# Optimization experiments

Measured on AMD Instinct MI355X. Metric: run time of the kernel, lower is better.

## Reference

```python
import jax, jax.numpy as jnp
import numpy as np

EPS = 1e-5  # RMSNorm epsilon


def rmsnorm(x, w):
    return x * jax.lax.rsqrt(jnp.mean(x * x, axis=-1, keepdims=True) + EPS) * w


def mamba_forward(u, in_proj_w, conv_w, conv_b, x_proj_w, dt_proj_w, dt_proj_b,
                  A_log, D_param, mamba_out_w):
    # u: (b, L, dm) -- canonical Mamba block (expand=2, d_state=16, d_conv=4)
    b, L, dm = u.shape
    di, ds = A_log.shape
    dtr = dt_proj_w.shape[1]
    xz = jnp.einsum('bld,ed->ble', u, in_proj_w)          # (b,L,2*di)
    x_, z = jnp.split(xz, 2, axis=-1)                     # each (b,L,di)
    # causal depthwise conv over the sequence axis
    dconv = conv_w.shape[-1]
    xc = jnp.transpose(x_, (0, 2, 1))                     # (b,di,L)
    xc = jnp.pad(xc, ((0, 0), (0, 0), (dconv - 1, 0)))
    xc = jax.lax.conv_general_dilated(xc, conv_w, window_strides=(1,), padding='VALID',
                                      dimension_numbers=('NCH', 'OIH', 'NCH'),
                                      feature_group_count=di)
    xc = xc + conv_b[None, :, None]
    x_ = jax.nn.silu(jnp.transpose(xc, (0, 2, 1)))        # (b,L,di)
    # input-dependent dt, B, C
    x_dbl = jnp.einsum('bld,ed->ble', x_, x_proj_w)       # (b,L,dtr+2*ds)
    dt, B, C = jnp.split(x_dbl, [dtr, dtr + ds], axis=-1)
    delta = jax.nn.softplus(jnp.einsum('blr,dr->bld', dt, dt_proj_w) + dt_proj_b)  # (b,L,di)
    A = -jnp.exp(A_log)                                   # (di,ds)

    def step(h, inp):
        d_t, B_t, C_t, x_t = inp                          # (b,di),(b,ds),(b,ds),(b,di)
        dA = jnp.exp(d_t[:, :, None] * A)                 # (b,di,ds)
        h = dA * h + (d_t * x_t)[:, :, None] * B_t[:, None, :]
        y = jnp.einsum('bds,bs->bd', h, C_t)
        return h, y

    xs = (jnp.moveaxis(delta, 1, 0), jnp.moveaxis(B, 1, 0),
          jnp.moveaxis(C, 1, 0), jnp.moveaxis(x_, 1, 0))
    h0 = jnp.zeros((b, di, ds), dtype=u.dtype)
    _, ys = jax.lax.scan(step, h0, xs)                    # ys: (L,b,di)
    y = jnp.moveaxis(ys, 0, 1) + x_ * D_param             # (b,L,di)
    y = y * jax.nn.silu(z)
    return jnp.einsum('bld,od->blo', y, mamba_out_w)      # (b,L,dm)


def conv1x1(W, bvec, t):
    # t: (b, cin, L) -> (b, cout, L)
    return jnp.einsum('oi,bit->bot', W, t) + bvec[None, :, None]


def reference(x, w_norm1, w_norm2, W_ip, b_ip, W_fp, b_fp, W_wp, b_wp, W_op, b_op,
              in_proj_w, conv_w, conv_b, x_proj_w, dt_proj_w, dt_proj_b,
              A_log, D_param, mamba_out_w):
    # x: (b, L, D) -- module's (b, c, l) with l == input_dim = D, c == seq = L
    residual = x
    xn = rmsnorm(x, w_norm1)                 # RMSNorm over last (input_dim) axis
    xt = jnp.transpose(xn, (0, 2, 1))        # 'b c l -> b l c' : (b, D, L)
    ssm = conv1x1(W_ip, b_ip, xt)            # (b, 2D, L)
    ssm = conv1x1(W_fp, b_fp, ssm)           # (b, 2D, L)
    u = jnp.transpose(ssm, (0, 2, 1))        # (b, L, 2D): seq=L, d_model=2D
    m = mamba_forward(u, in_proj_w, conv_w, conv_b, x_proj_w, dt_proj_w, dt_proj_b,
                      A_log, D_param, mamba_out_w)
    m = rmsnorm(m, w_norm2) + u              # PostNormMamba residual
    ssm = jnp.transpose(m, (0, 2, 1))        # (b, 2D, L)
    w = conv1x1(W_wp, b_wp, xt)              # (b, 2D, L)
    w = w * jax.nn.sigmoid(w)                # swish
    out = conv1x1(W_op, b_op, w * ssm)       # (b, D, L)
    return jnp.transpose(out, (0, 2, 1)) + residual


def setup_inputs():
    key = jax.random.key(0)
    ks = jax.random.split(key, 16)
    D, L, b = 64, 4096, 4
    dm, di, ds, dconv = 2 * D, 4 * D, 16, 4
    dtr = (dm + 15) // 16  # dt_rank = ceil(d_model/16) = 8

    def n(k, shape, fan_in):
        return jax.random.normal(k, shape, jnp.float32) * (1.0 / np.sqrt(fan_in))

    return {
        'x': jax.random.normal(ks[0], (b, L, D), jnp.float32),
        'w_norm1': jnp.ones((D,), jnp.float32),
        'w_norm2': jnp.ones((dm,), jnp.float32),
        'W_ip': n(ks[1], (2 * D, D), D), 'b_ip': jnp.zeros((2 * D,), jnp.float32),
        'W_fp': n(ks[2], (2 * D, 2 * D), 2 * D), 'b_fp': jnp.zeros((2 * D,), jnp.float32),
        'W_wp': n(ks[3], (2 * D, D), D), 'b_wp': jnp.zeros((2 * D,), jnp.float32),
        'W_op': n(ks[4], (D, 2 * D), 2 * D), 'b_op': jnp.zeros((D,), jnp.float32),
        'in_proj_w': n(ks[5], (2 * di, dm), dm),
        'conv_w': n(ks[6], (di, 1, dconv), dconv),
        'conv_b': jnp.zeros((di,), jnp.float32),
        'x_proj_w': n(ks[7], (dtr + 2 * ds, di), di),
        'dt_proj_w': n(ks[8], (di, dtr), dtr),
        'dt_proj_b': jnp.full((di,), float(np.log(np.expm1(0.01))), jnp.float32),
        'A_log': jnp.log(jnp.broadcast_to(jnp.arange(1, ds + 1, dtype=jnp.float32), (di, ds))),
        'D_param': jnp.ones((di,), jnp.float32),
        'mamba_out_w': n(ks[9], (dm, di), di),
    }
```

## Files before the change

kernel.cpp:

```cpp
#include <hip/hip_runtime.h>
#include <hip/hip_bf16.h>

typedef __hip_bfloat16 bf16;
typedef __attribute__((ext_vector_type(8))) short bf16x8;
typedef __attribute__((ext_vector_type(4))) float f32x4;
#define DEV __device__ __forceinline__

constexpr int SEQ  = 4096;
constexpr int NB   = 4;
constexpr int NTOK = NB * SEQ;
constexpr float EPS = 1e-5f;
constexpr int NCH = 64;
constexpr int NCHUNK = SEQ / NCH;
constexpr float LOG2E = 1.44269504f;

constexpr int OFF_WDT  = 0;
constexpr int OFF_WB   = 2048;
constexpr int WB_IP = 0;
constexpr int WB_WP = 8192;
constexpr int WB_FP = 16384;
constexpr int WB_PR = 32768;
constexpr int WB_MO = 98304;
constexpr int WB_OP = 131072;
constexpr int WB_XP = 139264;
constexpr int WB_TOT = 151552;
constexpr int OFF_XDBL = OFF_WB + WB_TOT / 2;
constexpr int OFF_R1   = OFF_XDBL + NTOK * 40;
constexpr int OFF_WSW  = OFF_R1   + 1048576;
constexpr int OFF_U    = OFF_WSW  + 1048576;
constexpr int OFF_R2   = OFF_U    + 1048576;
constexpr int OFF_SILUZ= OFF_R2   + 2097152;
constexpr int OFF_XC   = OFF_SILUZ+ 2097152;
constexpr int OFF_G    = OFF_XC   + 2097152;
constexpr int OFF_FLAG = OFF_G    + 2097152;

DEV float b2f(bf16 x) { return __bfloat162float(x); }
DEV bf16 f2b(float x) { return __float2bfloat16(x); }
DEV short shof(bf16 h) { short s; __builtin_memcpy(&s, &h, 2); return s; }
DEV float ldin(const void* p, int i, int f) {
  return f ? ((const float*)p)[i] : b2f(((const bf16*)p)[i]);
}
DEV unsigned pack2(float a, float b) {
  bf16 ha = f2b(a), hb = f2b(b);
  unsigned short ua, ub;
  __builtin_memcpy(&ua, &ha, 2); __builtin_memcpy(&ub, &hb, 2);
  return (unsigned)ua | ((unsigned)ub << 16);
}
DEV float lo16f(unsigned u) { return __int_as_float((int)(u << 16)); }
DEV float hi16f(unsigned u) { return __int_as_float((int)(u & 0xffff0000u)); }
template<int CTRL>
DEV float dpp_add(float v) {
  int r = __builtin_amdgcn_update_dpp(0, __float_as_int(v), CTRL, 0xF, 0xF, false);
  return v + __int_as_float(r);
}
DEV float exp2f_fast(float a) { return __builtin_amdgcn_exp2f(a); }
DEV float softplus(float a) {
  return (a > 20.f) ? a : __logf(1.f + exp2f_fast(a * LOG2E));
}
DEV float silu(float a) { return a / (1.f + __expf(-a)); }

DEV void cpw(int e, int base, int count, const void* __restrict__ src,
             bf16* __restrict__ wb, int f) {
  int r = e - base;
  if (r >= 0 && r < count) wb[base + r] = f2b(ldin(src, r, f));
}
__global__ __launch_bounds__(256) void prep_k(
    const void* __restrict__ w_ip, const void* __restrict__ w_wp, const void* __restrict__ w_fp,
    const void* __restrict__ w_pr, const void* __restrict__ w_mo, const void* __restrict__ w_op,
    const void* __restrict__ w_x,  const void* __restrict__ w_dt,
    const void* __restrict__ x, float* __restrict__ wsf, int* __restrict__ flagp)
{
  __shared__ int cnt;
  if (threadIdx.x == 0) cnt = 0;
  __syncthreads();
  {
    float v = b2f(((const bf16*)x)[threadIdx.x]);
    int ok = (v == v) && fabsf(v) > 1e-4f && fabsf(v) < 100.f;
    atomicAdd(&cnt, ok);
  }
  __syncthreads();
  int f = (cnt > 204) ? 0 : 1;
  if (blockIdx.x == 0 && threadIdx.x == 0) *flagp = f;

  int e = blockIdx.x * 256 + threadIdx.x;
  bf16* wb = (bf16*)(wsf + OFF_WB);
  cpw(e, WB_IP, 8192,  w_ip, wb, f);
  cpw(e, WB_WP, 8192,  w_wp, wb, f);
  cpw(e, WB_FP, 16384, w_fp, wb, f);
  cpw(e, WB_PR, 65536, w_pr, wb, f);
  cpw(e, WB_MO, 32768, w_mo, wb, f);
  cpw(e, WB_OP, 8192,  w_op, wb, f);
  {
    int r = e - WB_XP;
    if (r >= 0 && r < 12288) wb[WB_XP + r] = (r < 10240) ? f2b(ldin(w_x, r, f)) : f2b(0.f);
  }
  if (e < 2048) {
    int r = e >> 8, d = e & 255;
    wsf[OFF_WDT + e] = ldin(w_dt, d * 8 + r, f);
  }
}

__global__ __launch_bounds__(256) void fm_k(
    const void* __restrict__ x, const void* __restrict__ w1, const float* __restrict__ wsf,
    const void* __restrict__ b_ip, const void* __restrict__ b_wp, const void* __restrict__ b_fp,
    bf16* __restrict__ wsw, bf16* __restrict__ u, bf16* __restrict__ xpre,
    bf16* __restrict__ siluz, const int* __restrict__ flagp)
{
  __shared__ short xn[32 * 72];
  __shared__ short t1[32 * 136];
  __shared__ short ul[32 * 136];
  const int f = *flagp;
  const int tid = threadIdx.x;
  const int tok0 = blockIdx.x * 32;
  {
    const int token = tid >> 3, r = tid & 7;
    float v[8]; float ss = 0.f;
    #pragma unroll
    for (int k = 0; k < 8; ++k) {
      v[k] = ldin(x, (tok0 + token) * 64 + r * 8 + k, f);
      ss += v[k] * v[k];
    }
    ss += __shfl_xor(ss, 1, 8); ss += __shfl_xor(ss, 2, 8); ss += __shfl_xor(ss, 4, 8);
    float sc = rsqrtf(ss * (1.f / 64.f) + EPS);
    unsigned* dst = (unsigned*)xn + token * 36 + r * 4;
    #pragma unroll
    for (int k = 0; k < 4; ++k) {
      int i = r * 8 + k * 2;
      dst[k] = pack2(v[k*2] * sc * ldin(w1, i, f), v[k*2+1] * sc * ldin(w1, i + 1, f));
    }
  }
  __syncthreads();
  const int lane = tid & 63, m = lane & 15, q = lane >> 4;
  const int w = tid >> 6;
  {
    const int wt = w >> 1, ng = w & 1;
    const bf16* W = (const bf16*)(wsf + OFF_WB) + (wt ? WB_WP : WB_IP);
    const void* bia = wt ? b_wp : b_ip;
    bf16x8 a[2][2];
    #pragma unroll
    for (int mt = 0; mt < 2; ++mt)
      #pragma unroll
      for (int kk = 0; kk < 2; ++kk)
        a[mt][kk] = *(const bf16x8*)&xn[(mt * 16 + m) * 72 + kk * 32 + q * 8];
    #pragma unroll
    for (int nti = 0; nti < 4; ++nti) {
      int nt = ng * 4 + nti;
      int n = nt * 16 + m;
      f32x4 acc[2] = {{0,0,0,0},{0,0,0,0}};
      #pragma unroll
      for (int kk = 0; kk < 2; ++kk) {
        bf16x8 b = *(const bf16x8*)(W + (nt * 16 + m) * 64 + kk * 32 + q * 8);
        #pragma unroll
        for (int mt = 0; mt < 2; ++mt)
          acc[mt] = __builtin_amdgcn_mfma_f32_16x16x32_bf16(a[mt][kk], b, acc[mt], 0, 0, 0);
      }
      float bv = ldin(bia, n, f);
      #pragma unroll
      for (int mt = 0; mt < 2; ++mt)
        #pragma unroll
        for (int r = 0; r < 4; ++r) {
          float v = acc[mt][r] + bv;
          if (wt) wsw[(tok0 + mt * 16 + q * 4 + r) * 128 + n] = f2b(silu(v));
          else    t1[(mt * 16 + q * 4 + r) * 136 + n] = shof(f2b(v));
        }
    }
  }
  __syncthreads();
  {
    const bf16* WF = (const bf16*)(wsf + OFF_WB) + WB_FP;
    bf16x8 a[2][4];
    #pragma unroll
    for (int mt = 0; mt < 2; ++mt)
      #pragma unroll
      for (int kk = 0; kk < 4; ++kk)
        a[mt][kk] = *(const bf16x8*)&t1[(mt * 16 + m) * 136 + kk * 32 + q * 8];
    #pragma unroll
    for (int nti = 0; nti < 2; ++nti) {
      int nt = w * 2 + nti;
      int n = nt * 16 + m;
      f32x4 acc[2] = {{0,0,0,0},{0,0,0,0}};
      #pragma unroll
      for (int kk = 0; kk < 4; ++kk) {
        bf16x8 b = *(const bf16x8*)(WF + (nt * 16 + m) * 128 + kk * 32 + q * 8);
        #pragma unroll
        for (int mt = 0; mt < 2; ++mt)
          acc[mt] = __builtin_amdgcn_mfma_f32_16x16x32_bf16(a[mt][kk], b, acc[mt], 0, 0, 0);
      }
      float bv = ldin(b_fp, n, f);
      #pragma unroll
      for (int mt = 0; mt < 2; ++mt)
        #pragma unroll
        for (int r = 0; r < 4; ++r) {
          bf16 h = f2b(acc[mt][r] + bv);
          ul[(mt * 16 + q * 4 + r) * 136 + n] = shof(h);
          u[(tok0 + mt * 16 + q * 4 + r) * 128 + n] = h;
        }
    }
  }
  __syncthreads();
  {
    const bf16* WP = (const bf16*)(wsf + OFF_WB) + WB_PR;
    bf16x8 a[2][4];
    #pragma unroll
    for (int mt = 0; mt < 2; ++mt)
      #pragma unroll
      for (int kk = 0; kk < 4; ++kk)
        a[mt][kk] = *(const bf16x8*)&ul[(mt * 16 + m) * 136 + kk * 32 + q * 8];
    #pragma unroll
    for (int nti = 0; nti < 8; ++nti) {
      int nt = w * 8 + nti;
      int n = nt * 16 + m;
      f32x4 acc[2] = {{0,0,0,0},{0,0,0,0}};
      #pragma unroll
      for (int kk = 0; kk < 4; ++kk) {
        bf16x8 b = *(const bf16x8*)(WP + (nt * 16 + m) * 128 + kk * 32 + q * 8);
        #pragma unroll
        for (int mt = 0; mt < 2; ++mt)
          acc[mt] = __builtin_amdgcn_mfma_f32_16x16x32_bf16(a[mt][kk], b, acc[mt], 0, 0, 0);
      }
      #pragma unroll
      for (int mt = 0; mt < 2; ++mt)
        #pragma unroll
        for (int r = 0; r < 4; ++r) {
          int tok = tok0 + mt * 16 + q * 4 + r;
          if (n < 256) xpre[tok * 256 + n] = f2b(acc[mt][r]);
          else         siluz[tok * 256 + (n - 256)] = f2b(silu(acc[mt][r]));
        }
    }
  }
}

__global__ __launch_bounds__(256) void conv_k(
    const bf16* __restrict__ xpre, const void* __restrict__ cw, const void* __restrict__ cb,
    const float* __restrict__ wsf, bf16* __restrict__ xc, float* __restrict__ xdbl,
    const int* __restrict__ flagp)
{
  __shared__ short xh[35 * 256];
  __shared__ short cs[32 * 264];
  const int f = *flagp;
  const int tid = threadIdx.x;
  const int tok0 = blockIdx.x * 32;
  const bool seqstart = (tok0 & (SEQ - 1)) == 0;
  for (int c = tid; c < 1120; c += 256) {
    int e0 = c * 8;
    int tt = e0 >> 8, i = e0 & 255;
    int gtok = tok0 + tt - 3;
    uint4* dst = (uint4*)(xh + e0);
    if (gtok >= 0 && !(seqstart && tt < 3)) *dst = *(const uint4*)(xpre + gtok * 256 + i);
    else                                    *dst = make_uint4(0, 0, 0, 0);
  }
  __syncthreads();
  {
    const int ch0 = (tid & 63) * 4;
    const int t0 = (tid >> 6) * 8;
    float w4[4][4], cb4[4];
    #pragma unroll
    for (int c = 0; c < 4; ++c) {
      cb4[c] = ldin(cb, ch0 + c, f);
      #pragma unroll
      for (int k = 0; k < 4; ++k) w4[c][k] = ldin(cw, (ch0 + c) * 4 + k, f);
    }
    float win[11][4];
    #pragma unroll
    for (int r = 0; r < 11; ++r) {
      uint2 v = *(const uint2*)&xh[(t0 + r) * 256 + ch0];
      win[r][0] = lo16f(v.x); win[r][1] = hi16f(v.x);
      win[r][2] = lo16f(v.y); win[r][3] = hi16f(v.y);
    }
    #pragma unroll
    for (int t = 0; t < 8; ++t) {
      unsigned pk[2];
      #pragma unroll
      for (int cp = 0; cp < 2; ++cp) {
        float o[2];
        #pragma unroll
        for (int ci = 0; ci < 2; ++ci) {
          int c = cp * 2 + ci;
          float acc = cb4[c];
          #pragma unroll
          for (int k = 0; k < 4; ++k) acc = fmaf(win[t + k][c], w4[c][k], acc);
          o[ci] = silu(acc);
        }
        pk[cp] = pack2(o[0], o[1]);
      }
      uint2 pv = make_uint2(pk[0], pk[1]);
      *(uint2*)&cs[(t0 + t) * 264 + ch0] = pv;
      *(uint2*)(xc + (tok0 + t0 + t) * 256 + ch0) = pv;
    }
  }
  __syncthreads();
  const int w = tid >> 6;
  if (w < 2) {
    const bf16* Wx = (const bf16*)(wsf + OFF_WB) + WB_XP;
    const int lane = tid & 63, m = lane & 15, quad = lane >> 4;
    f32x4 acc[3] = {{0,0,0,0},{0,0,0,0},{0,0,0,0}};
    #pragma unroll
    for (int k0 = 0; k0 < 256; k0 += 32) {
      bf16x8 af = *(const bf16x8*)&cs[(w * 16 + m) * 264 + k0 + quad * 8];
      #pragma unroll
      for (int nt = 0; nt < 3; ++nt) {
        bf16x8 bfr = *(const bf16x8*)(Wx + (nt * 16 + m) * 256 + k0 + quad * 8);
        acc[nt] = __builtin_amdgcn_mfma_f32_16x16x32_bf16(af, bfr, acc[nt], 0, 0, 0);
      }
    }
    #pragma unroll
    for (int nt = 0; nt < 3; ++nt) {
      int n = nt * 16 + m;
      if (n < 40) {
        #pragma unroll
        for (int r = 0; r < 4; ++r)
          xdbl[(tok0 + w * 16 + quad * 4 + r) * 40 + n] = acc[nt][r];
      }
    }
  }
}

template<bool IS_C>
__global__ __launch_bounds__(256) void scan_k(
    const float* __restrict__ xdbl, const bf16* __restrict__ xc, const bf16* __restrict__ siluz,
    const void* __restrict__ A_log, const void* __restrict__ D_par, const void* __restrict__ dt_b,
    const float* __restrict__ WDT, float* __restrict__ summ, const float* __restrict__ hinit,
    bf16* __restrict__ g, const int* __restrict__ flagp)
{
  const int f = *flagp;
  const int tid = threadIdx.x;
  const int bb = blockIdx.x >> 4, dg = blockIdx.x & 15, c = blockIdx.y;
  const int dl = tid >> 4, s = tid & 15;
  const int j = s;
  const int d_loop = dg * 16 + dl;
  const int d_stg  = dg * 16 + j;
  const int tok_base = bb * SEQ + c * NCH;

  __shared__ float dt_l[NCH * 8];
  __shared__ float dx_l[NCH * 16 * 2];
  __shared__ float bc_l[IS_C ? NCH * 16 * 2 : NCH * 16];
  __shared__ float g_l[IS_C ? NCH * 16 : 1];

  const float Aval2 = -__expf(ldin(A_log, d_loop * 16 + s, f)) * LOG2E;
  const float Dp_stg = ldin(D_par, d_stg, f);
  const float dtb_j = ldin(dt_b, d_stg, f);
  float wdt[8];
  #pragma unroll
  for (int r = 0; r < 8; ++r) wdt[r] = WDT[r * 256 + d_stg];

  const int sidx = (blockIdx.x * NCHUNK + c) * 256 + tid;
  float h = IS_C ? hinit[sidx] : 0.f;
  float sdlt = 0.f;

  for (int e2 = tid * 4; e2 < NCH * 8; e2 += 1024)
    *(float4*)(dt_l + e2) = *(const float4*)(xdbl + (tok_base + (e2 >> 3)) * 40 + (e2 & 7));
  #pragma unroll
  for (int k = 0; k < 4; ++k) {
    int e = tid + k * 256;
    int t = e >> 4;
    int tok = tok_base + t;
    float B = xdbl[tok * 40 + 8 + j];
    if (IS_C) {
      bc_l[e * 2 + 0] = B;
      bc_l[e * 2 + 1] = xdbl[tok * 40 + 24 + j];
    } else bc_l[e] = B;
  }
  __syncthreads();
  #pragma unroll
  for (int k = 0; k < 4; ++k) {
    int e = tid + k * 256;
    int t = e >> 4;
    float a = dtb_j;
    #pragma unroll
    for (int r = 0; r < 8; ++r) a = fmaf(dt_l[t * 8 + r], wdt[r], a);
    float dlt = softplus(a);
    float xcv = b2f(xc[(tok_base + t) * 256 + d_stg]);
    *(float2*)(dx_l + e * 2) = make_float2(dlt, dlt * xcv);
  }
  __syncthreads();

  #pragma unroll 8
  for (int t = 0; t < NCH; ++t) {
    float2 dx = *(const float2*)(dx_l + (t * 16 + dl) * 2);
    float dA = exp2f_fast(dx.x * Aval2);
    if (!IS_C) sdlt += dx.x;
    if (IS_C) {
      float2 bc = *(const float2*)(bc_l + (t * 16 + s) * 2);
      h = fmaf(dA, h, dx.y * bc.x);
      float p = h * bc.y;
      p = dpp_add<0x121>(p);
      p = dpp_add<0x122>(p);
      p = dpp_add<0x124>(p);
      p = dpp_add<0x128>(p);
      if (s == 0) g_l[t * 16 + dl] = p;
    } else {
      h = fmaf(dA, h, dx.y * bc_l[t * 16 + s]);
    }
  }
  if (IS_C) {
    __syncthreads();
    #pragma unroll
    for (int k = 0; k < 4; ++k) {
      int e = tid + k * 256;
      int t = e >> 4;
      int tok = tok_base + t;
      float xcv = b2f(xc[tok * 256 + d_stg]);
      g[tok * 256 + d_stg] = f2b((g_l[e] + xcv * Dp_stg) * b2f(siluz[tok * 256 + d_stg]));
    }
  } else {
    *(float2*)(summ + sidx * 2) = make_float2(exp2f_fast(Aval2 * sdlt), h);
  }
}

__global__ __launch_bounds__(256) void scanB_k(const float* __restrict__ summ, float* __restrict__ hinit) {
  int bx = blockIdx.x, qq = threadIdx.x;
  float h = 0.f;
  for (int c0 = 0; c0 < NCHUNK; c0 += 16) {
    float2 sv[16];
    #pragma unroll
    for (int k = 0; k < 16; ++k)
      sv[k] = *(const float2*)(summ + ((bx * NCHUNK + c0 + k) * 256 + qq) * 2);
    #pragma unroll
    for (int k = 0; k < 16; ++k) {
      hinit[(bx * NCHUNK + c0 + k) * 256 + qq] = h;
      h = fmaf(sv[k].x, h, sv[k].y);
    }
  }
}

__global__ __launch_bounds__(256) void back_k(
    const bf16* __restrict__ g, const float* __restrict__ wsf, const void* __restrict__ w2,
    const bf16* __restrict__ u, const bf16* __restrict__ wsw, const void* __restrict__ b_op,
    const void* __restrict__ x, void* __restrict__ out, const int* __restrict__ flagp)
{
  __shared__ short ms[32 * 136];
  const int f = *flagp;
  const int tid = threadIdx.x;
  const int tok0 = blockIdx.x * 32;
  const int lane = tid & 63, m = lane & 15, q = lane >> 4;
  const int w = tid >> 6;
  const bf16* WM = (const bf16*)(wsf + OFF_WB) + WB_MO;
  const bf16* WO = (const bf16*)(wsf + OFF_WB) + WB_OP;
  {
    f32x4 acc[2][2] = {{{0,0,0,0},{0,0,0,0}},{{0,0,0,0},{0,0,0,0}}};
    #pragma unroll
    for (int kk = 0; kk < 8; ++kk) {
      bf16x8 a0 = *(const bf16x8*)(g + (tok0 + m) * 256 + kk * 32 + q * 8);
      bf16x8 a1 = *(const bf16x8*)(g + (tok0 + 16 + m) * 256 + kk * 32 + q * 8);
      #pragma unroll
      for (int nti = 0; nti < 2; ++nti) {
        int nt = w * 2 + nti;
        bf16x8 b = *(const bf16x8*)(WM + (nt * 16 + m) * 256 + kk * 32 + q * 8);
        acc[nti][0] = __builtin_amdgcn_mfma_f32_16x16x32_bf16(a0, b, acc[nti][0], 0, 0, 0);
        acc[nti][1] = __builtin_amdgcn_mfma_f32_16x16x32_bf16(a1, b, acc[nti][1], 0, 0, 0);
      }
    }
    #pragma unroll
    for (int nti = 0; nti < 2; ++nti) {
      int n = (w * 2 + nti) * 16 + m;
      #pragma unroll
      for (int mt = 0; mt < 2; ++mt)
        #pragma unroll
        for (int r = 0; r < 4; ++r)
          ms[(mt * 16 + q * 4 + r) * 136 + n] = shof(f2b(acc[nti][mt][r]));
    }
  }
  __syncthreads();
  {
    const int token = tid >> 3, r = tid & 7;
    float mv[16]; float ss = 0.f;
    #pragma unroll
    for (int k = 0; k < 16; ++k) {
      mv[k] = b2f(((const bf16*)ms)[token * 136 + r * 16 + k]);
      ss += mv[k] * mv[k];
    }
    ss += __shfl_xor(ss, 1, 8); ss += __shfl_xor(ss, 2, 8); ss += __shfl_xor(ss, 4, 8);
    float sc = rsqrtf(ss * (1.f / 128.f) + EPS);
    #pragma unroll
    for (int k = 0; k < 16; ++k) {
      int i = r * 16 + k;
      int ga = (tok0 + token) * 128 + i;
      float v = mv[k] * sc * ldin(w2, i, f) + b2f(u[ga]);
      ms[token * 136 + i] = shof(f2b(v * b2f(wsw[ga])));
    }
  }
  __syncthreads();
  {
    bf16x8 a[2][4];
    #pragma unroll
    for (int mt = 0; mt < 2; ++mt)
      #pragma unroll
      for (int kk = 0; kk < 4; ++kk)
        a[mt][kk] = *(const bf16x8*)&ms[(mt * 16 + m) * 136 + kk * 32 + q * 8];
    int nt = w;
    f32x4 acc[2] = {{0,0,0,0},{0,0,0,0}};
    #pragma unroll
    for (int kk = 0; kk < 4; ++kk) {
      bf16x8 b = *(const bf16x8*)(WO + (nt * 16 + m) * 128 + kk * 32 + q * 8);
      #pragma unroll
      for (int mt = 0; mt < 2; ++mt)
        acc[mt] = __builtin_amdgcn_mfma_f32_16x16x32_bf16(a[mt][kk], b, acc[mt], 0, 0, 0);
    }
    int n = nt * 16 + m;
    float bv = ldin(b_op, n, f);
    #pragma unroll
    for (int mt = 0; mt < 2; ++mt)
      #pragma unroll
      for (int r = 0; r < 4; ++r) {
        int token = tok0 + mt * 16 + q * 4 + r;
        float v = acc[mt][r] + bv + ldin(x, token * 64 + n, f);
        if (f) ((float*)out)[token * 64 + n] = v;
        else   ((bf16*)out)[token * 64 + n] = f2b(v);
      }
  }
}

extern "C" void kernel_launch(void* const* d_in, const int* in_sizes, int n_in,
                              void* d_out, int out_size, void* d_ws, size_t ws_size,
                              hipStream_t stream) {
  (void)in_sizes; (void)n_in; (void)out_size; (void)ws_size;
  const void* x        = d_in[0];
  const void* w_norm1  = d_in[1];
  const void* w_norm2  = d_in[2];
  const void* W_ip     = d_in[3];
  const void* b_ip     = d_in[4];
  const void* W_fp     = d_in[5];
  const void* b_fp     = d_in[6];
  const void* W_wp     = d_in[7];
  const void* b_wp     = d_in[8];
  const void* W_op     = d_in[9];
  const void* b_op     = d_in[10];
  const void* in_proj  = d_in[11];
  const void* conv_w   = d_in[12];
  const void* conv_b   = d_in[13];
  const void* x_proj   = d_in[14];
  const void* dt_projw = d_in[15];
  const void* dt_projb = d_in[16];
  const void* A_log    = d_in[17];
  const void* D_par    = d_in[18];
  const void* mo_w     = d_in[19];

  float* wsf    = (float*)d_ws;
  float* xdbl   = wsf + OFF_XDBL;
  float* hin    = wsf + OFF_R1;
  bf16*  wsw_b  = (bf16*)(wsf + OFF_WSW);
  bf16*  u_b    = (bf16*)(wsf + OFF_U);
  bf16*  xpre_b = (bf16*)(wsf + OFF_R2);
  float* summ   = wsf + OFF_R2;
  bf16*  siluz_b= (bf16*)(wsf + OFF_SILUZ);
  bf16*  xc_b   = (bf16*)(wsf + OFF_XC);
  bf16*  g_b    = (bf16*)(wsf + OFF_G);
  int*   flagp  = (int*)(wsf + OFF_FLAG);

  prep_k<<<dim3(592), dim3(256), 0, stream>>>(W_ip, W_wp, W_fp, in_proj, mo_w, W_op,
                                              x_proj, dt_projw, x, wsf, flagp);
  fm_k<<<dim3(NTOK / 32), dim3(256), 0, stream>>>(x, w_norm1, wsf, b_ip, b_wp, b_fp,
                                                  wsw_b, u_b, xpre_b, siluz_b, flagp);
  conv_k<<<dim3(NTOK / 32), dim3(256), 0, stream>>>(xpre_b, conv_w, conv_b, wsf, xc_b, xdbl, flagp);
  scan_k<false><<<dim3(64, NCHUNK), dim3(256), 0, stream>>>(xdbl, xc_b, siluz_b, A_log, D_par,
                                                            dt_projb, wsf + OFF_WDT, summ, hin, g_b, flagp);
  scanB_k<<<dim3(64), dim3(256), 0, stream>>>(summ, hin);
  scan_k<true><<<dim3(64, NCHUNK), dim3(256), 0, stream>>>(xdbl, xc_b, siluz_b, A_log, D_par,
                                                           dt_projb, wsf + OFF_WDT, summ, hin, g_b, flagp);
  back_k<<<dim3(NTOK / 32), dim3(256), 0, stream>>>(g_b, wsf, w_norm2, u_b, wsw_b, b_op, x, d_out, flagp);
}
```

Baseline: 208.4 us.

## Halve token tiles per block and fuse chunk-carry pass into scan via last-block atomic

The token-parallel kernels (fm_k, conv_k, back_k) now process 16 tokens per block instead of 32. This doubles the grid to 1024 blocks and cuts shared memory per block, to improve occupancy and load balance across CUs. The separate scanB_k launch is removed. Instead, the last scan_k<false> block per channel group, detected with an atomic counter plus threadfence, runs the sequential chunk-carry propagation, which saves one launch. In exchange, weight fragments are reused across fewer tokens, so weight traffic per token rises, and the serial carry loop now runs inside the tail of the scan kernel.

```diff
diff --git a/kernel.cpp b/kernel.cpp
--- a/kernel.cpp
+++ b/kernel.cpp
@@ -33,6 +33,7 @@
 constexpr int OFF_XC   = OFF_SILUZ+ 2097152;
 constexpr int OFF_G    = OFF_XC   + 2097152;
 constexpr int OFF_FLAG = OFF_G    + 2097152;
+constexpr int OFF_CNTS = OFF_FLAG + 1;
 
 DEV float b2f(bf16 x) { return __bfloat162float(x); }
 DEV bf16 f2b(float x) { return __float2bfloat16(x); }
@@ -68,7 +69,8 @@
     const void* __restrict__ w_ip, const void* __restrict__ w_wp, const void* __restrict__ w_fp,
     const void* __restrict__ w_pr, const void* __restrict__ w_mo, const void* __restrict__ w_op,
     const void* __restrict__ w_x,  const void* __restrict__ w_dt,
-    const void* __restrict__ x, float* __restrict__ wsf, int* __restrict__ flagp)
+    const void* __restrict__ x, float* __restrict__ wsf, int* __restrict__ flagp,
+    int* __restrict__ cnts)
 {
   __shared__ int cnt;
   if (threadIdx.x == 0) cnt = 0;
@@ -80,7 +82,10 @@
   }
   __syncthreads();
   int f = (cnt > 204) ? 0 : 1;
-  if (blockIdx.x == 0 && threadIdx.x == 0) *flagp = f;
+  if (blockIdx.x == 0) {
+    if (threadIdx.x == 0) *flagp = f;
+    if (threadIdx.x < 64) cnts[threadIdx.x] = 0;
+  }
 
   int e = blockIdx.x * 256 + threadIdx.x;
   bf16* wb = (bf16*)(wsf + OFF_WB);
@@ -106,28 +111,26 @@
     bf16* __restrict__ wsw, bf16* __restrict__ u, bf16* __restrict__ xpre,
     bf16* __restrict__ siluz, const int* __restrict__ flagp)
 {
-  __shared__ short xn[32 * 72];
-  __shared__ short t1[32 * 136];
-  __shared__ short ul[32 * 136];
+  __shared__ short xn[16 * 72];
+  __shared__ short t1[16 * 136];
+  __shared__ short ul[16 * 136];
   const int f = *flagp;
   const int tid = threadIdx.x;
-  const int tok0 = blockIdx.x * 32;
-  {
-    const int token = tid >> 3, r = tid & 7;
-    float v[8]; float ss = 0.f;
-    #pragma unroll
-    for (int k = 0; k < 8; ++k) {
-      v[k] = ldin(x, (tok0 + token) * 64 + r * 8 + k, f);
+  const int tok0 = blockIdx.x * 16;
+  {
+    const int token = tid >> 4, r = tid & 15;
+    float v[4]; float ss = 0.f;
+    #pragma unroll
+    for (int k = 0; k < 4; ++k) {
+      v[k] = ldin(x, (tok0 + token) * 64 + r * 4 + k, f);
       ss += v[k] * v[k];
     }
-    ss += __shfl_xor(ss, 1, 8); ss += __shfl_xor(ss, 2, 8); ss += __shfl_xor(ss, 4, 8);
+    ss += __shfl_xor(ss, 1, 16); ss += __shfl_xor(ss, 2, 16);
+    ss += __shfl_xor(ss, 4, 16); ss += __shfl_xor(ss, 8, 16);
     float sc = rsqrtf(ss * (1.f / 64.f) + EPS);
-    unsigned* dst = (unsigned*)xn + token * 36 + r * 4;
-    #pragma unroll
-    for (int k = 0; k < 4; ++k) {
-      int i = r * 8 + k * 2;
-      dst[k] = pack2(v[k*2] * sc * ldin(w1, i, f), v[k*2+1] * sc * ldin(w1, i + 1, f));
-    }
+    unsigned* dst = (unsigned*)xn + token * 36 + r * 2;
+    dst[0] = pack2(v[0] * sc * ldin(w1, r * 4 + 0, f), v[1] * sc * ldin(w1, r * 4 + 1, f));
+    dst[1] = pack2(v[2] * sc * ldin(w1, r * 4 + 2, f), v[3] * sc * ldin(w1, r * 4 + 3, f));
   }
   __syncthreads();
   const int lane = tid & 63, m = lane & 15, q = lane >> 4;
@@ -136,96 +139,78 @@
     const int wt = w >> 1, ng = w & 1;
     const bf16* W = (const bf16*)(wsf + OFF_WB) + (wt ? WB_WP : WB_IP);
     const void* bia = wt ? b_wp : b_ip;
-    bf16x8 a[2][2];
-    #pragma unroll
-    for (int mt = 0; mt < 2; ++mt)
-      #pragma unroll
-      for (int kk = 0; kk < 2; ++kk)
-        a[mt][kk] = *(const bf16x8*)&xn[(mt * 16 + m) * 72 + kk * 32 + q * 8];
+    bf16x8 a[2];
+    #pragma unroll
+    for (int kk = 0; kk < 2; ++kk)
+      a[kk] = *(const bf16x8*)&xn[m * 72 + kk * 32 + q * 8];
     #pragma unroll
     for (int nti = 0; nti < 4; ++nti) {
       int nt = ng * 4 + nti;
       int n = nt * 16 + m;
-      f32x4 acc[2] = {{0,0,0,0},{0,0,0,0}};
+      f32x4 acc = {0.f, 0.f, 0.f, 0.f};
       #pragma unroll
       for (int kk = 0; kk < 2; ++kk) {
         bf16x8 b = *(const bf16x8*)(W + (nt * 16 + m) * 64 + kk * 32 + q * 8);
-        #pragma unroll
-        for (int mt = 0; mt < 2; ++mt)
-          acc[mt] = __builtin_amdgcn_mfma_f32_16x16x32_bf16(a[mt][kk], b, acc[mt], 0, 0, 0);
+        acc = __builtin_amdgcn_mfma_f32_16x16x32_bf16(a[kk], b, acc, 0, 0, 0);
       }
       float bv = ldin(bia, n, f);
       #pragma unroll
-      for (int mt = 0; mt < 2; ++mt)
-        #pragma unroll
-        for (int r = 0; r < 4; ++r) {
-          float v = acc[mt][r] + bv;
-          if (wt) wsw[(tok0 + mt * 16 + q * 4 + r) * 128 + n] = f2b(silu(v));
-          else    t1[(mt * 16 + q * 4 + r) * 136 + n] = shof(f2b(v));
-        }
+      for (int r = 0; r < 4; ++r) {
+        float v = acc[r] + bv;
+        if (wt) wsw[(tok0 + q * 4 + r) * 128 + n] = f2b(silu(v));
+        else    t1[(q * 4 + r) * 136 + n] = shof(f2b(v));
+      }
     }
   }
   __syncthreads();
   {
     const bf16* WF = (const bf16*)(wsf + OFF_WB) + WB_FP;
-    bf16x8 a[2][4];
-    #pragma unroll
-    for (int mt = 0; mt < 2; ++mt)
-      #pragma unroll
-      for (int kk = 0; kk < 4; ++kk)
-        a[mt][kk] = *(const bf16x8*)&t1[(mt * 16 + m) * 136 + kk * 32 + q * 8];
+    bf16x8 a[4];
+    #pragma unroll
+    for (int kk = 0; kk < 4; ++kk)
+      a[kk] = *(const bf16x8*)&t1[m * 136 + kk * 32 + q * 8];
     #pragma unroll
     for (int nti = 0; nti < 2; ++nti) {
       int nt = w * 2 + nti;
       int n = nt * 16 + m;
-      f32x4 acc[2] = {{0,0,0,0},{0,0,0,0}};
+      f32x4 acc = {0.f, 0.f, 0.f, 0.f};
       #pragma unroll
       for (int kk = 0; kk < 4; ++kk) {
         bf16x8 b = *(const bf16x8*)(WF + (nt * 16 + m) * 128 + kk * 32 + q * 8);
-        #pragma unroll
-        for (int mt = 0; mt < 2; ++mt)
-          acc[mt] = __builtin_amdgcn_mfma_f32_16x16x32_bf16(a[mt][kk], b, acc[mt], 0, 0, 0);
+        acc = __builtin_amdgcn_mfma_f32_16x16x32_bf16(a[kk], b, acc, 0, 0, 0);
       }
       float bv = ldin(b_fp, n, f);
       #pragma unroll
-      for (int mt = 0; mt < 2; ++mt)
-        #pragma unroll
-        for (int r = 0; r < 4; ++r) {
-          bf16 h = f2b(acc[mt][r] + bv);
-          ul[(mt * 16 + q * 4 + r) * 136 + n] = shof(h);
-          u[(tok0 + mt * 16 + q * 4 + r) * 128 + n] = h;
-        }
+      for (int r = 0; r < 4; ++r) {
+        bf16 h = f2b(acc[r] + bv);
+        ul[(q * 4 + r) * 136 + n] = shof(h);
+        u[(tok0 + q * 4 + r) * 128 + n] = h;
+      }
     }
   }
   __syncthreads();
   {
     const bf16* WP = (const bf16*)(wsf + OFF_WB) + WB_PR;
-    bf16x8 a[2][4];
-    #pragma unroll
-    for (int mt = 0; mt < 2; ++mt)
-      #pragma unroll
-      for (int kk = 0; kk < 4; ++kk)
-        a[mt][kk] = *(const bf16x8*)&ul[(mt * 16 + m) * 136 + kk * 32 + q * 8];
+    bf16x8 a[4];
+    #pragma unroll
+    for (int kk = 0; kk < 4; ++kk)
+      a[kk] = *(const bf16x8*)&ul[m * 136 + kk * 32 + q * 8];
     #pragma unroll
     for (int nti = 0; nti < 8; ++nti) {
       int nt = w * 8 + nti;
       int n = nt * 16 + m;
-      f32x4 acc[2] = {{0,0,0,0},{0,0,0,0}};
+      f32x4 acc = {0.f, 0.f, 0.f, 0.f};
       #pragma unroll
       for (int kk = 0; kk < 4; ++kk) {
         bf16x8 b = *(const bf16x8*)(WP + (nt * 16 + m) * 128 + kk * 32 + q * 8);
-        #pragma unroll
-        for (int mt = 0; mt < 2; ++mt)
-          acc[mt] = __builtin_amdgcn_mfma_f32_16x16x32_bf16(a[mt][kk], b, acc[mt], 0, 0, 0);
-      }
-      #pragma unroll
-      for (int mt = 0; mt < 2; ++mt)
-        #pragma unroll
-        for (int r = 0; r < 4; ++r) {
-          int tok = tok0 + mt * 16 + q * 4 + r;
-          if (n < 256) xpre[tok * 256 + n] = f2b(acc[mt][r]);
-          else         siluz[tok * 256 + (n - 256)] = f2b(silu(acc[mt][r]));
-        }
+        acc = __builtin_amdgcn_mfma_f32_16x16x32_bf16(a[kk], b, acc, 0, 0, 0);
+      }
+      #pragma unroll
+      for (int r = 0; r < 4; ++r) {
+        int tok = tok0 + q * 4 + r;
+        if (n < 256) xpre[tok * 256 + n] = f2b(acc[r]);
+        else         siluz[tok * 256 + (n - 256)] = f2b(silu(acc[r]));
+      }
     }
   }
 }
@@ -235,13 +220,13 @@
     const float* __restrict__ wsf, bf16* __restrict__ xc, float* __restrict__ xdbl,
     const int* __restrict__ flagp)
 {
-  __shared__ short xh[35 * 256];
-  __shared__ short cs[32 * 264];
+  __shared__ short xh[19 * 256];
+  __shared__ short cs[16 * 264];
   const int f = *flagp;
   const int tid = threadIdx.x;
-  const int tok0 = blockIdx.x * 32;
+  const int tok0 = blockIdx.x * 16;
   const bool seqstart = (tok0 & (SEQ - 1)) == 0;
-  for (int c = tid; c < 1120; c += 256) {
+  for (int c = tid; c < 608; c += 256) {
     int e0 = c * 8;
     int tt = e0 >> 8, i = e0 & 255;
     int gtok = tok0 + tt - 3;
@@ -252,7 +237,7 @@
   __syncthreads();
   {
     const int ch0 = (tid & 63) * 4;
-    const int t0 = (tid >> 6) * 8;
+    const int t0 = (tid >> 6) * 4;
     float w4[4][4], cb4[4];
     #pragma unroll
     for (int c = 0; c < 4; ++c) {
@@ -260,15 +245,15 @@
       #pragma unroll
       for (int k = 0; k < 4; ++k) w4[c][k] = ldin(cw, (ch0 + c) * 4 + k, f);
     }
-    float win[11][4];
-    #pragma unroll
-    for (int r = 0; r < 11; ++r) {
+    float win[7][4];
+    #pragma unroll
+    for (int r = 0; r < 7; ++r) {
       uint2 v = *(const uint2*)&xh[(t0 + r) * 256 + ch0];
       win[r][0] = lo16f(v.x); win[r][1] = hi16f(v.x);
       win[r][2] = lo16f(v.y); win[r][3] = hi16f(v.y);
     }
     #pragma unroll
-    for (int t = 0; t < 8; ++t) {
+    for (int t = 0; t < 4; ++t) {
       unsigned pk[2];
       #pragma unroll
       for (int cp = 0; cp < 2; ++cp) {
@@ -290,27 +275,21 @@
   }
   __syncthreads();
   const int w = tid >> 6;
-  if (w < 2) {
+  if (w < 3) {
     const bf16* Wx = (const bf16*)(wsf + OFF_WB) + WB_XP;
     const int lane = tid & 63, m = lane & 15, quad = lane >> 4;
-    f32x4 acc[3] = {{0,0,0,0},{0,0,0,0},{0,0,0,0}};
+    f32x4 acc = {0.f, 0.f, 0.f, 0.f};
     #pragma unroll
     for (int k0 = 0; k0 < 256; k0 += 32) {
-      bf16x8 af = *(const bf16x8*)&cs[(w * 16 + m) * 264 + k0 + quad * 8];
-      #pragma unroll
-      for (int nt = 0; nt < 3; ++nt) {
-        bf16x8 bfr = *(const bf16x8*)(Wx + (nt * 16 + m) * 256 + k0 + quad * 8);
-        acc[nt] = __builtin_amdgcn_mfma_f32_16x16x32_bf16(af, bfr, acc[nt], 0, 0, 0);
-      }
-    }
-    #pragma unroll
-    for (int nt = 0; nt < 3; ++nt) {
-      int n = nt * 16 + m;
-      if (n < 40) {
-        #pragma unroll
-        for (int r = 0; r < 4; ++r)
-          xdbl[(tok0 + w * 16 + quad * 4 + r) * 40 + n] = acc[nt][r];
-      }
+      bf16x8 af = *(const bf16x8*)&cs[m * 264 + k0 + quad * 8];
+      bf16x8 bfr = *(const bf16x8*)(Wx + (w * 16 + m) * 256 + k0 + quad * 8);
+      acc = __builtin_amdgcn_mfma_f32_16x16x32_bf16(af, bfr, acc, 0, 0, 0);
+    }
+    int n = w * 16 + m;
+    if (n < 40) {
+      #pragma unroll
+      for (int r = 0; r < 4; ++r)
+        xdbl[(tok0 + quad * 4 + r) * 40 + n] = acc[r];
     }
   }
 }
@@ -319,8 +298,8 @@
 __global__ __launch_bounds__(256) void scan_k(
     const float* __restrict__ xdbl, const bf16* __restrict__ xc, const bf16* __restrict__ siluz,
     const void* __restrict__ A_log, const void* __restrict__ D_par, const void* __restrict__ dt_b,
-    const float* __restrict__ WDT, float* __restrict__ summ, const float* __restrict__ hinit,
-    bf16* __restrict__ g, const int* __restrict__ flagp)
+    const float* __restrict__ WDT, float* __restrict__ summ, float* __restrict__ hinit,
+    bf16* __restrict__ g, const int* __restrict__ flagp, int* __restrict__ cnts)
 {
   const int f = *flagp;
   const int tid = threadIdx.x;
@@ -335,6 +314,7 @@
   __shared__ float dx_l[NCH * 16 * 2];
   __shared__ float bc_l[IS_C ? NCH * 16 * 2 : NCH * 16];
   __shared__ float g_l[IS_C ? NCH * 16 : 1];
+  __shared__ int lastf;
 
   const float Aval2 = -__expf(ldin(A_log, d_loop * 16 + s, f)) * LOG2E;
   const float Dp_stg = ldin(D_par, d_stg, f);
@@ -404,21 +384,25 @@
     }
   } else {
     *(float2*)(summ + sidx * 2) = make_float2(exp2f_fast(Aval2 * sdlt), h);
-  }
-}
-
-__global__ __launch_bounds__(256) void scanB_k(const float* __restrict__ summ, float* __restrict__ hinit) {
-  int bx = blockIdx.x, qq = threadIdx.x;
-  float h = 0.f;
-  for (int c0 = 0; c0 < NCHUNK; c0 += 16) {
-    float2 sv[16];
-    #pragma unroll
-    for (int k = 0; k < 16; ++k)
-      sv[k] = *(const float2*)(summ + ((bx * NCHUNK + c0 + k) * 256 + qq) * 2);
-    #pragma unroll
-    for (int k = 0; k < 16; ++k) {
-      hinit[(bx * NCHUNK + c0 + k) * 256 + qq] = h;
-      h = fmaf(sv[k].x, h, sv[k].y);
+    __threadfence();
+    if (tid == 0)
+      lastf = (atomicAdd(&cnts[blockIdx.x], 1) == NCHUNK - 1) ? 1 : 0;
+    __syncthreads();
+    if (lastf) {
+      __threadfence();
+      const int bx = blockIdx.x;
+      float h2 = 0.f;
+      for (int c0 = 0; c0 < NCHUNK; c0 += 16) {
+        float2 sv[16];
+        #pragma unroll
+        for (int k = 0; k < 16; ++k)
+          sv[k] = *(const float2*)(summ + ((bx * NCHUNK + c0 + k) * 256 + tid) * 2);
+        #pragma unroll
+        for (int k = 0; k < 16; ++k) {
+          hinit[(bx * NCHUNK + c0 + k) * 256 + tid] = h2;
+          h2 = fmaf(sv[k].x, h2, sv[k].y);
+        }
+      }
     }
   }
 }
@@ -428,52 +412,49 @@
     const bf16* __restrict__ u, const bf16* __restrict__ wsw, const void* __restrict__ b_op,
     const void* __restrict__ x, void* __restrict__ out, const int* __restrict__ flagp)
 {
-  __shared__ short ms[32 * 136];
+  __shared__ short ms[16 * 136];
   const int f = *flagp;
   const int tid = threadIdx.x;
-  const int tok0 = blockIdx.x * 32;
+  const int tok0 = blockIdx.x * 16;
   const int lane = tid & 63, m = lane & 15, q = lane >> 4;
   const int w = tid >> 6;
   const bf16* WM = (const bf16*)(wsf + OFF_WB) + WB_MO;
   const bf16* WO = (const bf16*)(wsf + OFF_WB) + WB_OP;
   {
-    f32x4 acc[2][2] = {{{0,0,0,0},{0,0,0,0}},{{0,0,0,0},{0,0,0,0}}};
+    f32x4 acc[2] = {{0,0,0,0},{0,0,0,0}};
     #pragma unroll
     for (int kk = 0; kk < 8; ++kk) {
       bf16x8 a0 = *(const bf16x8*)(g + (tok0 + m) * 256 + kk * 32 + q * 8);
-      bf16x8 a1 = *(const bf16x8*)(g + (tok0 + 16 + m) * 256 + kk * 32 + q * 8);
       #pragma unroll
       for (int nti = 0; nti < 2; ++nti) {
         int nt = w * 2 + nti;
         bf16x8 b = *(const bf16x8*)(WM + (nt * 16 + m) * 256 + kk * 32 + q * 8);
-        acc[nti][0] = __builtin_amdgcn_mfma_f32_16x16x32_bf16(a0, b, acc[nti][0], 0, 0, 0);
-        acc[nti][1] = __builtin_amdgcn_mfma_f32_16x16x32_bf16(a1, b, acc[nti][1], 0, 0, 0);
+        acc[nti] = __builtin_amdgcn_mfma_f32_16x16x32_bf16(a0, b, acc[nti], 0, 0, 0);
       }
     }
     #pragma unroll
     for (int nti = 0; nti < 2; ++nti) {
       int n = (w * 2 + nti) * 16 + m;
       #pragma unroll
-      for (int mt = 0; mt < 2; ++mt)
-        #pragma unroll
-        for (int r = 0; r < 4; ++r)
-          ms[(mt * 16 + q * 4 + r) * 136 + n] = shof(f2b(acc[nti][mt][r]));
-    }
-  }
-  __syncthreads();
-  {
-    const int token = tid >> 3, r = tid & 7;
-    float mv[16]; float ss = 0.f;
-    #pragma unroll
-    for (int k = 0; k < 16; ++k) {
-      mv[k] = b2f(((const bf16*)ms)[token * 136 + r * 16 + k]);
+      for (int r = 0; r < 4; ++r)
+        ms[(q * 4 + r) * 136 + n] = shof(f2b(acc[nti][r]));
+    }
+  }
+  __syncthreads();
+  {
+    const int token = tid >> 4, r = tid & 15;
+    float mv[8]; float ss = 0.f;
+    #pragma unroll
+    for (int k = 0; k < 8; ++k) {
+      mv[k] = b2f(((const bf16*)ms)[token * 136 + r * 8 + k]);
       ss += mv[k] * mv[k];
     }
-    ss += __shfl_xor(ss, 1, 8); ss += __shfl_xor(ss, 2, 8); ss += __shfl_xor(ss, 4, 8);
+    ss += __shfl_xor(ss, 1, 16); ss += __shfl_xor(ss, 2, 16);
+    ss += __shfl_xor(ss, 4, 16); ss += __shfl_xor(ss, 8, 16);
     float sc = rsqrtf(ss * (1.f / 128.f) + EPS);
     #pragma unroll
-    for (int k = 0; k < 16; ++k) {
-      int i = r * 16 + k;
+    for (int k = 0; k < 8; ++k) {
+      int i = r * 8 + k;
       int ga = (tok0 + token) * 128 + i;
       float v = mv[k] * sc * ldin(w2, i, f) + b2f(u[ga]);
       ms[token * 136 + i] = shof(f2b(v * b2f(wsw[ga])));
@@ -481,32 +462,25 @@
   }
   __syncthreads();
   {
-    bf16x8 a[2][4];
-    #pragma unroll
-    for (int mt = 0; mt < 2; ++mt)
-      #pragma unroll
-      for (int kk = 0; kk < 4; ++kk)
-        a[mt][kk] = *(const bf16x8*)&ms[(mt * 16 + m) * 136 + kk * 32 + q * 8];
-    int nt = w;
-    f32x4 acc[2] = {{0,0,0,0},{0,0,0,0}};
+    bf16x8 a[4];
+    #pragma unroll
+    for (int kk = 0; kk < 4; ++kk)
+      a[kk] = *(const bf16x8*)&ms[m * 136 + kk * 32 + q * 8];
+    f32x4 acc = {0.f, 0.f, 0.f, 0.f};
     #pragma unroll
     for (int kk = 0; kk < 4; ++kk) {
-      bf16x8 b = *(const bf16x8*)(WO + (nt * 16 + m) * 128 + kk * 32 + q * 8);
-      #pragma unroll
-      for (int mt = 0; mt < 2; ++mt)
-        acc[mt] = __builtin_amdgcn_mfma_f32_16x16x32_bf16(a[mt][kk], b, acc[mt], 0, 0, 0);
-    }
-    int n = nt * 16 + m;
+      bf16x8 b = *(const bf16x8*)(WO + (w * 16 + m) * 128 + kk * 32 + q * 8);
+      acc = __builtin_amdgcn_mfma_f32_16x16x32_bf16(a[kk], b, acc, 0, 0, 0);
+    }
+    int n = w * 16 + m;
     float bv = ldin(b_op, n, f);
     #pragma unroll
-    for (int mt = 0; mt < 2; ++mt)
-      #pragma unroll
-      for (int r = 0; r < 4; ++r) {
-        int token = tok0 + mt * 16 + q * 4 + r;
-        float v = acc[mt][r] + bv + ldin(x, token * 64 + n, f);
-        if (f) ((float*)out)[token * 64 + n] = v;
-        else   ((bf16*)out)[token * 64 + n] = f2b(v);
-      }
+    for (int r = 0; r < 4; ++r) {
+      int token = tok0 + q * 4 + r;
+      float v = acc[r] + bv + ldin(x, token * 64 + n, f);
+      if (f) ((float*)out)[token * 64 + n] = v;
+      else   ((bf16*)out)[token * 64 + n] = f2b(v);
+    }
   }
 }
 
@@ -546,16 +520,16 @@
   bf16*  xc_b   = (bf16*)(wsf + OFF_XC);
   bf16*  g_b    = (bf16*)(wsf + OFF_G);
   int*   flagp  = (int*)(wsf + OFF_FLAG);
+  int*   cnts   = (int*)(wsf + OFF_CNTS);
 
   prep_k<<<dim3(592), dim3(256), 0, stream>>>(W_ip, W_wp, W_fp, in_proj, mo_w, W_op,
-                                              x_proj, dt_projw, x, wsf, flagp);
-  fm_k<<<dim3(NTOK / 32), dim3(256), 0, stream>>>(x, w_norm1, wsf, b_ip, b_wp, b_fp,
+                                              x_proj, dt_projw, x, wsf, flagp, cnts);
+  fm_k<<<dim3(NTOK / 16), dim3(256), 0, stream>>>(x, w_norm1, wsf, b_ip, b_wp, b_fp,
                                                   wsw_b, u_b, xpre_b, siluz_b, flagp);
-  conv_k<<<dim3(NTOK / 32), dim3(256), 0, stream>>>(xpre_b, conv_w, conv_b, wsf, xc_b, xdbl, flagp);
+  conv_k<<<dim3(NTOK / 16), dim3(256), 0, stream>>>(xpre_b, conv_w, conv_b, wsf, xc_b, xdbl, flagp);
   scan_k<false><<<dim3(64, NCHUNK), dim3(256), 0, stream>>>(xdbl, xc_b, siluz_b, A_log, D_par,
-                                                            dt_projb, wsf + OFF_WDT, summ, hin, g_b, flagp);
-  scanB_k<<<dim3(64), dim3(256), 0, stream>>>(summ, hin);
+                                                            dt_projb, wsf + OFF_WDT, summ, hin, g_b, flagp, cnts);
   scan_k<true><<<dim3(64, NCHUNK), dim3(256), 0, stream>>>(xdbl, xc_b, siluz_b, A_log, D_par,
-                                                           dt_projb, wsf + OFF_WDT, summ, hin, g_b, flagp);
-  back_k<<<dim3(NTOK / 32), dim3(256), 0, stream>>>(g_b, wsf, w_norm2, u_b, wsw_b, b_op, x, d_out, flagp);
-}
+                                                           dt_projb, wsf + OFF_WDT, summ, hin, g_b, flagp, cnts);
+  back_k<<<dim3(NTOK / 16), dim3(256), 0, stream>>>(g_b, wsf, w_norm2, u_b, wsw_b, b_op, x, d_out, flagp);
+}
```

Measured after the change: 551.6 us. +164.7%, slower.

## Restructure chunked scan to one thread per channel holding all 16 states

Applied to the files above, without the earlier changes.

The scan kernels now map each thread to one inner channel and keep all 16 state values in registers, instead of one thread per (channel, state) pair. This removes the DPP cross-lane reduction for the C·h output and the g_l staging, and computes delta once per channel rather than redundantly. Blocks shrink to 64 threads with 16x64 grid, and the chunk-summary layout and scanB indexing change to match. The trade-off is fewer threads, 1024 per chunk pass, giving lower occupancy and more serial per-thread work, plus higher register pressure.

```diff
diff --git a/kernel.cpp b/kernel.cpp
--- a/kernel.cpp
+++ b/kernel.cpp
@@ -48,11 +48,6 @@
 }
 DEV float lo16f(unsigned u) { return __int_as_float((int)(u << 16)); }
 DEV float hi16f(unsigned u) { return __int_as_float((int)(u & 0xffff0000u)); }
-template<int CTRL>
-DEV float dpp_add(float v) {
-  int r = __builtin_amdgcn_update_dpp(0, __float_as_int(v), CTRL, 0xF, 0xF, false);
-  return v + __int_as_float(r);
-}
 DEV float exp2f_fast(float a) { return __builtin_amdgcn_exp2f(a); }
 DEV float softplus(float a) {
   return (a > 20.f) ? a : __logf(1.f + exp2f_fast(a * LOG2E));
@@ -316,108 +311,129 @@
 }
 
 template<bool IS_C>
-__global__ __launch_bounds__(256) void scan_k(
+__global__ __launch_bounds__(64) void scan_k(
     const float* __restrict__ xdbl, const bf16* __restrict__ xc, const bf16* __restrict__ siluz,
     const void* __restrict__ A_log, const void* __restrict__ D_par, const void* __restrict__ dt_b,
     const float* __restrict__ WDT, float* __restrict__ summ, const float* __restrict__ hinit,
     bf16* __restrict__ g, const int* __restrict__ flagp)
 {
+  __shared__ float dt_l[NCH * 8];
+  __shared__ float B_l[NCH * 16];
+  __shared__ float C_l[IS_C ? NCH * 16 : 4];
+  __shared__ float dlt_l[NCH * 64];
   const int f = *flagp;
   const int tid = threadIdx.x;
-  const int bb = blockIdx.x >> 4, dg = blockIdx.x & 15, c = blockIdx.y;
-  const int dl = tid >> 4, s = tid & 15;
-  const int j = s;
-  const int d_loop = dg * 16 + dl;
-  const int d_stg  = dg * 16 + j;
+  const int bb = blockIdx.x >> 2, dg = blockIdx.x & 3;
+  const int c = blockIdx.y;
+  const int d = dg * 64 + tid;
   const int tok_base = bb * SEQ + c * NCH;
 
-  __shared__ float dt_l[NCH * 8];
-  __shared__ float dx_l[NCH * 16 * 2];
-  __shared__ float bc_l[IS_C ? NCH * 16 * 2 : NCH * 16];
-  __shared__ float g_l[IS_C ? NCH * 16 : 1];
-
-  const float Aval2 = -__expf(ldin(A_log, d_loop * 16 + s, f)) * LOG2E;
-  const float Dp_stg = ldin(D_par, d_stg, f);
-  const float dtb_j = ldin(dt_b, d_stg, f);
+  float A2[16], h[16];
+  #pragma unroll
+  for (int s = 0; s < 16; ++s)
+    A2[s] = -__expf(ldin(A_log, d * 16 + s, f)) * LOG2E;
+  const float Dp = ldin(D_par, d, f);
+  const float dtb = ldin(dt_b, d, f);
   float wdt[8];
   #pragma unroll
-  for (int r = 0; r < 8; ++r) wdt[r] = WDT[r * 256 + d_stg];
-
-  const int sidx = (blockIdx.x * NCHUNK + c) * 256 + tid;
-  float h = IS_C ? hinit[sidx] : 0.f;
+  for (int r = 0; r < 8; ++r) wdt[r] = WDT[r * 256 + d];
+
+  {
+    const float4* src = (const float4*)(xdbl + (tok_base + tid) * 40);
+    *(float4*)(dt_l + tid * 8)      = src[0];
+    *(float4*)(dt_l + tid * 8 + 4)  = src[1];
+    #pragma unroll
+    for (int k = 0; k < 4; ++k)
+      *(float4*)(B_l + tid * 16 + k * 4) = src[2 + k];
+    if (IS_C) {
+      #pragma unroll
+      for (int k = 0; k < 4; ++k)
+        *(float4*)(C_l + tid * 16 + k * 4) = src[6 + k];
+    }
+  }
+  __syncthreads();
+
+  for (int t = 0; t < NCH; ++t) {
+    float4 d0 = *(const float4*)(dt_l + t * 8);
+    float4 d1 = *(const float4*)(dt_l + t * 8 + 4);
+    float a = dtb;
+    a = fmaf(d0.x, wdt[0], a); a = fmaf(d0.y, wdt[1], a);
+    a = fmaf(d0.z, wdt[2], a); a = fmaf(d0.w, wdt[3], a);
+    a = fmaf(d1.x, wdt[4], a); a = fmaf(d1.y, wdt[5], a);
+    a = fmaf(d1.z, wdt[6], a); a = fmaf(d1.w, wdt[7], a);
+    dlt_l[t * 64 + tid] = softplus(a);
+  }
+  __syncthreads();
+
+  #pragma unroll
+  for (int s = 0; s < 16; ++s) h[s] = 0.f;
+  if (IS_C) {
+    const int hbase = (bb * 64 + c) * 4096 + d * 16;
+    #pragma unroll
+    for (int k = 0; k < 4; ++k)
+      *(float4*)(h + k * 4) = *(const float4*)(hinit + hbase + k * 4);
+  }
   float sdlt = 0.f;
 
-  for (int e2 = tid * 4; e2 < NCH * 8; e2 += 1024)
-    *(float4*)(dt_l + e2) = *(const float4*)(xdbl + (tok_base + (e2 >> 3)) * 40 + (e2 & 7));
-  #pragma unroll
-  for (int k = 0; k < 4; ++k) {
-    int e = tid + k * 256;
-    int t = e >> 4;
-    int tok = tok_base + t;
-    float B = xdbl[tok * 40 + 8 + j];
+  #pragma unroll 4
+  for (int t = 0; t < NCH; ++t) {
+    float dlt = dlt_l[t * 64 + tid];
+    float xcv = b2f(xc[(tok_base + t) * 256 + d]);
+    float du = dlt * xcv;
+    float Bv[16];
+    #pragma unroll
+    for (int k = 0; k < 4; ++k)
+      *(float4*)(Bv + k * 4) = *(const float4*)(B_l + t * 16 + k * 4);
     if (IS_C) {
-      bc_l[e * 2 + 0] = B;
-      bc_l[e * 2 + 1] = xdbl[tok * 40 + 24 + j];
-    } else bc_l[e] = B;
-  }
-  __syncthreads();
-  #pragma unroll
-  for (int k = 0; k < 4; ++k) {
-    int e = tid + k * 256;
-    int t = e >> 4;
-    float a = dtb_j;
-    #pragma unroll
-    for (int r = 0; r < 8; ++r) a = fmaf(dt_l[t * 8 + r], wdt[r], a);
-    float dlt = softplus(a);
-    float xcv = b2f(xc[(tok_base + t) * 256 + d_stg]);
-    *(float2*)(dx_l + e * 2) = make_float2(dlt, dlt * xcv);
-  }
-  __syncthreads();
-
-  #pragma unroll 8
-  for (int t = 0; t < NCH; ++t) {
-    float2 dx = *(const float2*)(dx_l + (t * 16 + dl) * 2);
-    float dA = exp2f_fast(dx.x * Aval2);
-    if (!IS_C) sdlt += dx.x;
-    if (IS_C) {
-      float2 bc = *(const float2*)(bc_l + (t * 16 + s) * 2);
-      h = fmaf(dA, h, dx.y * bc.x);
-      float p = h * bc.y;
-      p = dpp_add<0x121>(p);
-      p = dpp_add<0x122>(p);
-      p = dpp_add<0x124>(p);
-      p = dpp_add<0x128>(p);
-      if (s == 0) g_l[t * 16 + dl] = p;
+      float Cv[16];
+      #pragma unroll
+      for (int k = 0; k < 4; ++k)
+        *(float4*)(Cv + k * 4) = *(const float4*)(C_l + t * 16 + k * 4);
+      float y = 0.f;
+      #pragma unroll
+      for (int s = 0; s < 16; ++s) {
+        float dA = exp2f_fast(dlt * A2[s]);
+        h[s] = fmaf(dA, h[s], du * Bv[s]);
+        y = fmaf(h[s], Cv[s], y);
+      }
+      float sz = b2f(siluz[(tok_base + t) * 256 + d]);
+      g[(tok_base + t) * 256 + d] = f2b((y + xcv * Dp) * sz);
     } else {
-      h = fmaf(dA, h, dx.y * bc_l[t * 16 + s]);
-    }
-  }
-  if (IS_C) {
-    __syncthreads();
-    #pragma unroll
-    for (int k = 0; k < 4; ++k) {
-      int e = tid + k * 256;
-      int t = e >> 4;
-      int tok = tok_base + t;
-      float xcv = b2f(xc[tok * 256 + d_stg]);
-      g[tok * 256 + d_stg] = f2b((g_l[e] + xcv * Dp_stg) * b2f(siluz[tok * 256 + d_stg]));
-    }
-  } else {
-    *(float2*)(summ + sidx * 2) = make_float2(exp2f_fast(Aval2 * sdlt), h);
+      sdlt += dlt;
+      #pragma unroll
+      for (int s = 0; s < 16; ++s) {
+        float dA = exp2f_fast(dlt * A2[s]);
+        h[s] = fmaf(dA, h[s], du * Bv[s]);
+      }
+    }
+  }
+  if (!IS_C) {
+    float sv[32];
+    #pragma unroll
+    for (int s = 0; s < 16; ++s) {
+      sv[s * 2]     = exp2f_fast(A2[s] * sdlt);
+      sv[s * 2 + 1] = h[s];
+    }
+    float* dst = summ + ((bb * 64 + c) * 4096 + d * 16) * 2;
+    #pragma unroll
+    for (int k = 0; k < 8; ++k)
+      *(float4*)(dst + k * 4) = *(const float4*)(sv + k * 4);
   }
 }
 
 __global__ __launch_bounds__(256) void scanB_k(const float* __restrict__ summ, float* __restrict__ hinit) {
-  int bx = blockIdx.x, qq = threadIdx.x;
+  int bx = blockIdx.x;
+  int b = bx >> 4;
+  int q = (bx & 15) * 256 + threadIdx.x;
   float h = 0.f;
   for (int c0 = 0; c0 < NCHUNK; c0 += 16) {
     float2 sv[16];
     #pragma unroll
     for (int k = 0; k < 16; ++k)
-      sv[k] = *(const float2*)(summ + ((bx * NCHUNK + c0 + k) * 256 + qq) * 2);
+      sv[k] = *(const float2*)(summ + ((b * 64 + c0 + k) * 4096 + q) * 2);
     #pragma unroll
     for (int k = 0; k < 16; ++k) {
-      hinit[(bx * NCHUNK + c0 + k) * 256 + qq] = h;
+      hinit[(b * 64 + c0 + k) * 4096 + q] = h;
       h = fmaf(sv[k].x, h, sv[k].y);
     }
   }
@@ -552,10 +568,10 @@
   fm_k<<<dim3(NTOK / 32), dim3(256), 0, stream>>>(x, w_norm1, wsf, b_ip, b_wp, b_fp,
                                                   wsw_b, u_b, xpre_b, siluz_b, flagp);
   conv_k<<<dim3(NTOK / 32), dim3(256), 0, stream>>>(xpre_b, conv_w, conv_b, wsf, xc_b, xdbl, flagp);
-  scan_k<false><<<dim3(64, NCHUNK), dim3(256), 0, stream>>>(xdbl, xc_b, siluz_b, A_log, D_par,
-                                                            dt_projb, wsf + OFF_WDT, summ, hin, g_b, flagp);
+  scan_k<false><<<dim3(16, NCHUNK), dim3(64), 0, stream>>>(xdbl, xc_b, siluz_b, A_log, D_par,
+                                                           dt_projb, wsf + OFF_WDT, summ, hin, g_b, flagp);
   scanB_k<<<dim3(64), dim3(256), 0, stream>>>(summ, hin);
-  scan_k<true><<<dim3(64, NCHUNK), dim3(256), 0, stream>>>(xdbl, xc_b, siluz_b, A_log, D_par,
-                                                           dt_projb, wsf + OFF_WDT, summ, hin, g_b, flagp);
+  scan_k<true><<<dim3(16, NCHUNK), dim3(64), 0, stream>>>(xdbl, xc_b, siluz_b, A_log, D_par,
+                                                          dt_projb, wsf + OFF_WDT, summ, hin, g_b, flagp);
   back_k<<<dim3(NTOK / 32), dim3(256), 0, stream>>>(g_b, wsf, w_norm2, u_b, wsw_b, b_op, x, d_out, flagp);
 }
```

Result: no change. 209.6 us (+0.6%).
